# Performance work log

Measured on AMD Instinct MI355X. Metric: run time of the kernel, lower is better.

The kernel has to match this reference:

```python
import jax, jax.numpy as jnp
import numpy as np

E = 500000          # num edges
N = 50000           # num nodes
D_IN = 32           # n_input_features (edge feature dim)
D_HID = 128         # n_hidden_features
D_NODE = 16         # n_node_features; MLP head outputs D_NODE**2


def _linear_params(key, d_in, d_out):
    kw, kb = jax.random.split(key)
    bound = 1.0 / np.sqrt(d_in)
    W = jax.random.uniform(kw, (d_out, d_in), jnp.float32, -bound, bound)
    b = jax.random.uniform(kb, (d_out,), jnp.float32, -bound, bound)
    return W, b


def setup_inputs() -> dict:
    key = jax.random.key(0)
    k1, k2, k3, k4, k5, k6, k7 = jax.random.split(key, 7)
    edge_features = jax.random.normal(k1, (E, D_IN), jnp.float32)
    node_features = jax.random.normal(k2, (N, D_NODE), jnp.float32)
    edge_index = jax.random.randint(k3, (E, 2), 0, N, jnp.int64 if jax.config.jax_enable_x64 else jnp.int32)
    W1, b1 = _linear_params(k4, D_IN, D_HID)
    W2, b2 = _linear_params(k5, D_HID, D_HID)
    W3, b3 = _linear_params(k6, D_HID, D_HID)
    W4, b4 = _linear_params(k7, D_HID, D_NODE * D_NODE)
    return {
        "edge_features": edge_features,
        "node_features": node_features,
        "W1": W1, "b1": b1, "W2": W2, "b2": b2,
        "W3": W3, "b3": b3, "W4": W4, "b4": b4,
        "edge_index": edge_index,
    }


def reference(edge_features, node_features, W1, b1, W2, b2, W3, b3, W4, b4, edge_index):
    neighbors = edge_index[:, 1]                       # [E]
    ef = edge_features[neighbors]                      # [E, D_IN] gather
    nf = node_features[neighbors]                      # [E, D_NODE] gather
    h = jax.nn.relu(ef @ W1.T + b1)                    # [E, D_HID]
    h = jax.nn.relu(h @ W2.T + b2)
    h = jax.nn.relu(h @ W3.T + b3)
    edge_out = h @ W4.T + b4                           # [E, D_NODE**2]
    d = nf.shape[-1]
    message = edge_out.reshape(-1, d, d)               # [E, d, d]
    # per-edge matrix-vector product: (message @ nf[..., None]).squeeze(-1)
    return jnp.einsum("eij,ej->ei", message, nf)       # [E, d]
```

## Files before the change

### kernel.cpp

```cpp
#include <hip/hip_runtime.h>
#include <stdint.h>

typedef __attribute__((ext_vector_type(8))) short short8;
typedef __attribute__((ext_vector_type(4))) float f32x4;
typedef __attribute__((ext_vector_type(4))) unsigned int u32x4;

#define NE 500000
#define NN 50000
#define NTILES 3125
#define NPAIRS 1563

__device__ __forceinline__ unsigned int f2bf1(float f) {
  unsigned int u = __builtin_bit_cast(unsigned int, f);
  u += 0x7FFFu + ((u >> 16) & 1u);
  return u >> 16;
}
__device__ __forceinline__ unsigned int packbf2(float lo, float hi) {
  return f2bf1(lo) | (f2bf1(hi) << 16);
}
__device__ __forceinline__ short8 pack8(f32x4 a, f32x4 b) {
  short8 r;
  r[0] = (short)f2bf1(a[0]); r[1] = (short)f2bf1(a[1]);
  r[2] = (short)f2bf1(a[2]); r[3] = (short)f2bf1(a[3]);
  r[4] = (short)f2bf1(b[0]); r[5] = (short)f2bf1(b[1]);
  r[6] = (short)f2bf1(b[2]); r[7] = (short)f2bf1(b[3]);
  return r;
}

__global__ __launch_bounds__(256) void prep_weights(
    const float* __restrict__ W1, const float* __restrict__ W2,
    const float* __restrict__ W3, const float* __restrict__ W4,
    unsigned short* __restrict__ wf) {
  int t = blockIdx.x * 256 + threadIdx.x;
  if (t >= 136 * 64) return;
  int f = t >> 6, l = t & 63;
  const float* W; int K, nb, kf;
  if (f < 8)       { W = W1; K = 32;  kf = 0;            nb = f;      }
  else if (f < 40) { W = W2; K = 128; int i = f - 8;  kf = i >> 3; nb = i & 7;  }
  else if (f < 72) { W = W3; K = 128; int i = f - 40; kf = i >> 3; nb = i & 7;  }
  else             { W = W4; K = 128; int i = f - 72; kf = i >> 4; nb = i & 15; }
  const float* src = W + (nb * 16 + (l & 15)) * K + kf * 32 + (l >> 4) * 8;
  f32x4 x0 = *(const f32x4*)src;
  f32x4 x1 = *(const f32x4*)(src + 4);
  *(short8*)(wf + f * 512 + l * 8) = pack8(x0, x1);
}

__global__ __launch_bounds__(512, 2) void mlp_kernel(
    const float* __restrict__ ef, const float* __restrict__ nfeat,
    const float* __restrict__ b1, const float* __restrict__ b2,
    const float* __restrict__ b3, const float* __restrict__ b4,
    const unsigned short* __restrict__ wf, float* __restrict__ Rout) {
  __shared__ __align__(16) unsigned short wlds[36864];
  __shared__ __align__(16) float blds[640];
  __shared__ __align__(16) unsigned short hlds[8][2][2048];

  const int t = threadIdx.x;
  {
    const u32x4* src = (const u32x4*)wf;
    u32x4* dst = (u32x4*)wlds;
    #pragma unroll
    for (int i = 0; i < 9; ++i) dst[t + i * 512] = src[t + i * 512];
  }
  if (t < 160) {
    const float* s = t < 32 ? b1 + t * 4
                   : t < 64 ? b2 + (t - 32) * 4
                   : t < 96 ? b3 + (t - 64) * 4
                   :          b4 + (t - 96) * 4;
    ((f32x4*)blds)[t] = *(const f32x4*)s;
  }
  __syncthreads();

  const int lane = t & 63, w = t >> 6;
  const int l15 = lane & 15, lg = lane >> 4;
  char* hbA = (char*)&hlds[w][0][0];
  char* hbB = (char*)&hlds[w][1][0];
  const int swz = (l15 & 7) << 4;

  const int p = blockIdx.x * 8 + w;
  if (p >= NPAIRS) return;
  const int tA = 2 * p, tB = 2 * p + 1;
  const bool actB = (tB < NTILES);
  const int nA = tA * 16, nB = (actB ? tB : tA) * 16;

  auto trans_store = [&](const f32x4* a, char* hb) {
    #pragma unroll
    for (int nb = 0; nb < 8; ++nb) {
      float v0 = fmaxf(a[nb][0], 0.f), v1 = fmaxf(a[nb][1], 0.f);
      float v2 = fmaxf(a[nb][2], 0.f), v3 = fmaxf(a[nb][3], 0.f);
      unsigned long long dw = (unsigned long long)packbf2(v0, v1)
                            | ((unsigned long long)packbf2(v2, v3) << 32);
      int byte = (l15 * 256 + (nb * 16 + lg * 4) * 2) ^ swz;
      *(unsigned long long*)(hb + byte) = dw;
    }
  };
  auto trans_load = [&](short8* af, char* hb) {
    #pragma unroll
    for (int kf = 0; kf < 4; ++kf) {
      int byte = (l15 * 256 + kf * 64 + lg * 16) ^ swz;
      af[kf] = *(const short8*)(hb + byte);
    }
  };

  const float* xa = ef + (nA + l15) * 32 + lg * 8;
  const float* xb = ef + (nB + l15) * 32 + lg * 8;
  short8 a1A = pack8(*(const f32x4*)xa, *(const f32x4*)(xa + 4));
  short8 a1B = pack8(*(const f32x4*)xb, *(const f32x4*)(xb + 4));
  f32x4 accA[8], accB[8];
  #pragma unroll
  for (int nb = 0; nb < 8; ++nb) {
    f32x4 c0 = *(const f32x4*)&blds[nb * 16 + lg * 4];
    short8 wv = *(const short8*)&wlds[nb * 512 + lane * 8];
    accA[nb] = __builtin_amdgcn_mfma_f32_16x16x32_bf16(wv, a1A, c0, 0, 0, 0);
    accB[nb] = __builtin_amdgcn_mfma_f32_16x16x32_bf16(wv, a1B, c0, 0, 0, 0);
  }
  short8 afA[4], afB[4];
  trans_store(accA, hbA); trans_store(accB, hbB);
  asm volatile("s_waitcnt lgkmcnt(0)" ::: "memory");
  __builtin_amdgcn_sched_barrier(0);
  trans_load(afA, hbA); trans_load(afB, hbB);
  asm volatile("s_waitcnt lgkmcnt(0)" ::: "memory");
  __builtin_amdgcn_sched_barrier(0);

  #pragma unroll
  for (int L = 0; L < 2; ++L) {
    const int wbase = 8 + L * 32, bbase = 128 + L * 128;
    #pragma unroll
    for (int nb = 0; nb < 8; ++nb) {
      f32x4 c0 = *(const f32x4*)&blds[bbase + nb * 16 + lg * 4];
      f32x4 cA = c0, cB = c0;
      #pragma unroll
      for (int kf = 0; kf < 4; ++kf) {
        short8 wv = *(const short8*)&wlds[(wbase + kf * 8 + nb) * 512 + lane * 8];
        cA = __builtin_amdgcn_mfma_f32_16x16x32_bf16(wv, afA[kf], cA, 0, 0, 0);
        cB = __builtin_amdgcn_mfma_f32_16x16x32_bf16(wv, afB[kf], cB, 0, 0, 0);
      }
      accA[nb] = cA; accB[nb] = cB;
    }
    trans_store(accA, hbA); trans_store(accB, hbB);
    asm volatile("s_waitcnt lgkmcnt(0)" ::: "memory");
    __builtin_amdgcn_sched_barrier(0);
    trans_load(afA, hbA); trans_load(afB, hbB);
    asm volatile("s_waitcnt lgkmcnt(0)" ::: "memory");
    __builtin_amdgcn_sched_barrier(0);
  }

  const short8* w4 = (const short8*)(wf + 72 * 512);
  f32x4 nfvA = *(const f32x4*)(nfeat + (nA + l15) * 16 + lg * 4);
  f32x4 nfvB = *(const f32x4*)(nfeat + (nB + l15) * 16 + lg * 4);
  float oA0 = 0.f, oA1 = 0.f, oA2 = 0.f, oA3 = 0.f;
  float oB0 = 0.f, oB1 = 0.f, oB2 = 0.f, oB3 = 0.f;
  #pragma unroll
  for (int nb = 0; nb < 16; ++nb) {
    f32x4 c0 = *(const f32x4*)&blds[384 + nb * 16 + lg * 4];
    f32x4 dA = c0, dB = c0;
    #pragma unroll
    for (int kf = 0; kf < 4; ++kf) {
      short8 wv = w4[(kf * 16 + nb) * 64 + lane];
      dA = __builtin_amdgcn_mfma_f32_16x16x32_bf16(wv, afA[kf], dA, 0, 0, 0);
      dB = __builtin_amdgcn_mfma_f32_16x16x32_bf16(wv, afB[kf], dB, 0, 0, 0);
    }
    float pA = dA[0] * nfvA[0] + dA[1] * nfvA[1] + dA[2] * nfvA[2] + dA[3] * nfvA[3];
    float pB = dB[0] * nfvB[0] + dB[1] * nfvB[1] + dB[2] * nfvB[2] + dB[3] * nfvB[3];
    pA += __shfl_xor(pA, 16, 64); pA += __shfl_xor(pA, 32, 64);
    pB += __shfl_xor(pB, 16, 64); pB += __shfl_xor(pB, 32, 64);
    int rs = nb - lg * 4;
    oA0 = (rs == 0) ? pA : oA0; oA1 = (rs == 1) ? pA : oA1;
    oA2 = (rs == 2) ? pA : oA2; oA3 = (rs == 3) ? pA : oA3;
    oB0 = (rs == 0) ? pB : oB0; oB1 = (rs == 1) ? pB : oB1;
    oB2 = (rs == 2) ? pB : oB2; oB3 = (rs == 3) ? pB : oB3;
  }
  f32x4 oA = { oA0, oA1, oA2, oA3 };
  *(f32x4*)(Rout + (nA + l15) * 16 + lg * 4) = oA;
  if (actB) {
    f32x4 oB = { oB0, oB1, oB2, oB3 };
    *(f32x4*)(Rout + (nB + l15) * 16 + lg * 4) = oB;
  }
}

__global__ __launch_bounds__(256) void scatter_kernel(
    const int* __restrict__ eidx, const float* __restrict__ Rbuf,
    float* __restrict__ out) {
  int tid = blockIdx.x * 256 + threadIdx.x;
  const int total = NE * 4;
  const int stride = gridDim.x * 256;
  for (; tid < total; tid += stride) {
    int e = tid >> 2, p = tid & 3;
    int nb = eidx[2 * e + 1];
    f32x4 v = *(const f32x4*)(Rbuf + nb * 16 + p * 4);
    *(f32x4*)(out + e * 16 + p * 4) = v;
  }
}

extern "C" void kernel_launch(void* const* d_in, const int* in_sizes, int n_in,
                              void* d_out, int out_size, void* d_ws, size_t ws_size,
                              hipStream_t stream) {
  const float* ef = (const float*)d_in[0];
  const float* nf = (const float*)d_in[1];
  const float* W1 = (const float*)d_in[2];
  const float* b1 = (const float*)d_in[3];
  const float* W2 = (const float*)d_in[4];
  const float* b2 = (const float*)d_in[5];
  const float* W3 = (const float*)d_in[6];
  const float* b3 = (const float*)d_in[7];
  const float* W4 = (const float*)d_in[8];
  const float* b4 = (const float*)d_in[9];
  const int* eidx = (const int*)d_in[10];

  unsigned short* wf = (unsigned short*)d_ws;
  float* Rbuf = (float*)((char*)d_ws + 139264);
  float* out = (float*)d_out;

  hipLaunchKernelGGL(prep_weights, dim3(34), dim3(256), 0, stream, W1, W2, W3, W4, wf);
  hipLaunchKernelGGL(mlp_kernel, dim3(196), dim3(512), 0, stream,
                     ef, nf, b1, b2, b3, b4, wf, Rbuf);
  hipLaunchKernelGGL(scatter_kernel, dim3(2048), dim3(256), 0, stream, eidx, Rbuf, out);
}
```

Measured before the change: 37.67 us.

## Fuse weight prep into MLP kernel, keep activations in registers, stage W4 in LDS

Drops the separate weight-prep launch: each MLP block now converts fp32 weights to bf16 fragments straight into a larger LDS buffer that also holds W4. The layer-to-layer relu/pack transition moves from an LDS round trip to a register permutation, using a permuted K ordering that matches how the weights are laid out. The scatter uses nontemporal stores and the MLP grid grows to 256 blocks. In exchange every block redoes the weight conversion, and the larger LDS footprint may reduce occupancy.

Result: faster. 36.28 us (-3.7%).

```diff
diff --git a/kernel.cpp b/kernel.cpp
--- a/kernel.cpp
+++ b/kernel.cpp
@@ -27,39 +27,38 @@
   return r;
 }
 
-__global__ __launch_bounds__(256) void prep_weights(
-    const float* __restrict__ W1, const float* __restrict__ W2,
-    const float* __restrict__ W3, const float* __restrict__ W4,
-    unsigned short* __restrict__ wf) {
-  int t = blockIdx.x * 256 + threadIdx.x;
-  if (t >= 136 * 64) return;
-  int f = t >> 6, l = t & 63;
-  const float* W; int K, nb, kf;
-  if (f < 8)       { W = W1; K = 32;  kf = 0;            nb = f;      }
-  else if (f < 40) { W = W2; K = 128; int i = f - 8;  kf = i >> 3; nb = i & 7;  }
-  else if (f < 72) { W = W3; K = 128; int i = f - 40; kf = i >> 3; nb = i & 7;  }
-  else             { W = W4; K = 128; int i = f - 72; kf = i >> 4; nb = i & 15; }
-  const float* src = W + (nb * 16 + (l & 15)) * K + kf * 32 + (l >> 4) * 8;
-  f32x4 x0 = *(const f32x4*)src;
-  f32x4 x1 = *(const f32x4*)(src + 4);
-  *(short8*)(wf + f * 512 + l * 8) = pack8(x0, x1);
-}
-
 __global__ __launch_bounds__(512, 2) void mlp_kernel(
     const float* __restrict__ ef, const float* __restrict__ nfeat,
-    const float* __restrict__ b1, const float* __restrict__ b2,
-    const float* __restrict__ b3, const float* __restrict__ b4,
-    const unsigned short* __restrict__ wf, float* __restrict__ Rout) {
-  __shared__ __align__(16) unsigned short wlds[36864];
+    const float* __restrict__ W1, const float* __restrict__ b1,
+    const float* __restrict__ W2, const float* __restrict__ b2,
+    const float* __restrict__ W3, const float* __restrict__ b3,
+    const float* __restrict__ W4, const float* __restrict__ b4,
+    float* __restrict__ Rout) {
+  __shared__ __align__(16) unsigned short wlds[69632];
   __shared__ __align__(16) float blds[640];
-  __shared__ __align__(16) unsigned short hlds[8][2][2048];
 
   const int t = threadIdx.x;
-  {
-    const u32x4* src = (const u32x4*)wf;
-    u32x4* dst = (u32x4*)wlds;
-    #pragma unroll
-    for (int i = 0; i < 9; ++i) dst[t + i * 512] = src[t + i * 512];
+  #pragma unroll
+  for (int i = 0; i < 17; ++i) {
+    int idx = t + i * 512;
+    int f = idx >> 6, l = idx & 63;
+    int c2 = l & 15, g = l >> 4;
+    const float *pa, *pb;
+    if (f < 8) {
+      const float* base = W1 + (f * 16 + c2) * 32 + g * 8;
+      pa = base; pb = base + 4;
+    } else {
+      const float* W; int i2, kfq, nb;
+      if (f < 40)      { W = W2; i2 = f - 8;  kfq = i2 >> 3; nb = i2 & 7;  }
+      else if (f < 72) { W = W3; i2 = f - 40; kfq = i2 >> 3; nb = i2 & 7;  }
+      else             { W = W4; i2 = f - 72; kfq = i2 >> 4; nb = i2 & 15; }
+      const float* base = W + (nb * 16 + c2) * 128 + g * 4;
+      pa = base + kfq * 16;
+      pb = base + (kfq + 4) * 16;
+    }
+    f32x4 x0 = *(const f32x4*)pa;
+    f32x4 x1 = *(const f32x4*)pb;
+    *(short8*)&wlds[f * 512 + l * 8] = pack8(x0, x1);
   }
   if (t < 160) {
     const float* s = t < 32 ? b1 + t * 4
@@ -72,9 +71,6 @@
 
   const int lane = t & 63, w = t >> 6;
   const int l15 = lane & 15, lg = lane >> 4;
-  char* hbA = (char*)&hlds[w][0][0];
-  char* hbB = (char*)&hlds[w][1][0];
-  const int swz = (l15 & 7) << 4;
 
   const int p = blockIdx.x * 8 + w;
   if (p >= NPAIRS) return;
@@ -82,22 +78,17 @@
   const bool actB = (tB < NTILES);
   const int nA = tA * 16, nB = (actB ? tB : tA) * 16;
 
-  auto trans_store = [&](const f32x4* a, char* hb) {
+  auto transition = [&](const f32x4* a, short8* af) {
+    unsigned int pk[8][2];
     #pragma unroll
     for (int nb = 0; nb < 8; ++nb) {
-      float v0 = fmaxf(a[nb][0], 0.f), v1 = fmaxf(a[nb][1], 0.f);
-      float v2 = fmaxf(a[nb][2], 0.f), v3 = fmaxf(a[nb][3], 0.f);
-      unsigned long long dw = (unsigned long long)packbf2(v0, v1)
-                            | ((unsigned long long)packbf2(v2, v3) << 32);
-      int byte = (l15 * 256 + (nb * 16 + lg * 4) * 2) ^ swz;
-      *(unsigned long long*)(hb + byte) = dw;
+      pk[nb][0] = packbf2(fmaxf(a[nb][0], 0.f), fmaxf(a[nb][1], 0.f));
+      pk[nb][1] = packbf2(fmaxf(a[nb][2], 0.f), fmaxf(a[nb][3], 0.f));
     }
-  };
-  auto trans_load = [&](short8* af, char* hb) {
     #pragma unroll
     for (int kf = 0; kf < 4; ++kf) {
-      int byte = (l15 * 256 + kf * 64 + lg * 16) ^ swz;
-      af[kf] = *(const short8*)(hb + byte);
+      u32x4 u = { pk[kf][0], pk[kf][1], pk[kf + 4][0], pk[kf + 4][1] };
+      af[kf] = __builtin_bit_cast(short8, u);
     }
   };
 
@@ -114,12 +105,8 @@
     accB[nb] = __builtin_amdgcn_mfma_f32_16x16x32_bf16(wv, a1B, c0, 0, 0, 0);
   }
   short8 afA[4], afB[4];
-  trans_store(accA, hbA); trans_store(accB, hbB);
-  asm volatile("s_waitcnt lgkmcnt(0)" ::: "memory");
-  __builtin_amdgcn_sched_barrier(0);
-  trans_load(afA, hbA); trans_load(afB, hbB);
-  asm volatile("s_waitcnt lgkmcnt(0)" ::: "memory");
-  __builtin_amdgcn_sched_barrier(0);
+  transition(accA, afA);
+  transition(accB, afB);
 
   #pragma unroll
   for (int L = 0; L < 2; ++L) {
@@ -136,15 +123,10 @@
       }
       accA[nb] = cA; accB[nb] = cB;
     }
-    trans_store(accA, hbA); trans_store(accB, hbB);
-    asm volatile("s_waitcnt lgkmcnt(0)" ::: "memory");
-    __builtin_amdgcn_sched_barrier(0);
-    trans_load(afA, hbA); trans_load(afB, hbB);
-    asm volatile("s_waitcnt lgkmcnt(0)" ::: "memory");
-    __builtin_amdgcn_sched_barrier(0);
+    transition(accA, afA);
+    transition(accB, afB);
   }
 
-  const short8* w4 = (const short8*)(wf + 72 * 512);
   f32x4 nfvA = *(const f32x4*)(nfeat + (nA + l15) * 16 + lg * 4);
   f32x4 nfvB = *(const f32x4*)(nfeat + (nB + l15) * 16 + lg * 4);
   float oA0 = 0.f, oA1 = 0.f, oA2 = 0.f, oA3 = 0.f;
@@ -155,7 +137,7 @@
     f32x4 dA = c0, dB = c0;
     #pragma unroll
     for (int kf = 0; kf < 4; ++kf) {
-      short8 wv = w4[(kf * 16 + nb) * 64 + lane];
+      short8 wv = *(const short8*)&wlds[(72 + kf * 16 + nb) * 512 + lane * 8];
       dA = __builtin_amdgcn_mfma_f32_16x16x32_bf16(wv, afA[kf], dA, 0, 0, 0);
       dB = __builtin_amdgcn_mfma_f32_16x16x32_bf16(wv, afB[kf], dB, 0, 0, 0);
     }
@@ -187,7 +169,7 @@
     int e = tid >> 2, p = tid & 3;
     int nb = eidx[2 * e + 1];
     f32x4 v = *(const f32x4*)(Rbuf + nb * 16 + p * 4);
-    *(f32x4*)(out + e * 16 + p * 4) = v;
+    __builtin_nontemporal_store(v, (f32x4*)(out + e * 16 + p * 4));
   }
 }
 
@@ -206,12 +188,10 @@
   const float* b4 = (const float*)d_in[9];
   const int* eidx = (const int*)d_in[10];
 
-  unsigned short* wf = (unsigned short*)d_ws;
-  float* Rbuf = (float*)((char*)d_ws + 139264);
+  float* Rbuf = (float*)d_ws;
   float* out = (float*)d_out;
 
-  hipLaunchKernelGGL(prep_weights, dim3(34), dim3(256), 0, stream, W1, W2, W3, W4, wf);
-  hipLaunchKernelGGL(mlp_kernel, dim3(196), dim3(512), 0, stream,
-                     ef, nf, b1, b2, b3, b4, wf, Rbuf);
+  hipLaunchKernelGGL(mlp_kernel, dim3(256), dim3(512), 0, stream,
+                     ef, nf, W1, b1, W2, b2, W3, b3, W4, b4, Rbuf);
   hipLaunchKernelGGL(scatter_kernel, dim3(2048), dim3(256), 0, stream, eidx, Rbuf, out);
 }
```
